# Kernel optimization log

Hardware: AMD Instinct MI355X
Metric: run time of the kernel (lower is better)

Reference implementation:

```python
import jax, jax.numpy as jnp
import numpy as np

# Model dims (DeepSeek-V2-lite style MLA)
B, T, DIM = 1, 2048, 2048
H = 16
NOPE, ROPE, VD = 128, 64, 128
QKD = NOPE + ROPE            # 192
Q_LORA, KV_LORA = 768, 512
EPS = 1e-6
SOFTSCALE = QKD * -0.5       # faithful to source: qk_head_dim * -0.5 == -96.0 (NOT **-0.5)


def rms_norm(x, w):
    # F.rms_norm: x / sqrt(mean(x^2) + eps) * w
    return x * jax.lax.rsqrt(jnp.mean(x * x, axis=-1, keepdims=True) + EPS) * w


def apply_rope(x, freqs):
    # x: [B, T, H, D] with D even; freqs: [T, D//2] rotation angles.
    # Complex-pair rotation on interleaved (even, odd) pairs, DeepSeek style.
    b, t, h, d = x.shape
    xr = x.reshape(b, t, h, d // 2, 2)
    cos = jnp.cos(freqs)[None, :, None, :]
    sin = jnp.sin(freqs)[None, :, None, :]
    x1, x2 = xr[..., 0], xr[..., 1]
    out = jnp.stack([x1 * cos - x2 * sin, x1 * sin + x2 * cos], axis=-1)
    return out.reshape(b, t, h, d)


def setup_inputs() -> dict:
    key = jax.random.key(0)
    ks = jax.random.split(key, 8)

    def w(k, out_f, in_f):
        return jax.random.normal(k, (out_f, in_f), dtype=jnp.float32) * (in_f ** -0.5)

    x = jax.random.normal(ks[0], (B, T, DIM), dtype=jnp.float32)

    # RoPE angles: positions x inv_freq, [T, ROPE//2]
    inv_freq = 1.0 / (10000.0 ** (np.arange(0, ROPE, 2, dtype=np.float32) / ROPE))
    freqs = jnp.asarray(np.outer(np.arange(T, dtype=np.float32), inv_freq))

    # additive causal mask [T, T]
    mask = jnp.where(np.tril(np.ones((T, T), dtype=bool)), 0.0, -jnp.inf).astype(jnp.float32)

    return {
        "x": x,
        "freqs": freqs,
        "mask": mask,
        "wq_a": w(ks[1], Q_LORA, DIM),
        "q_norm_w": jnp.ones((Q_LORA,), dtype=jnp.float32),
        "wq_b": w(ks[2], H * QKD, Q_LORA),
        "wkv_a": w(ks[3], KV_LORA + ROPE, DIM),
        "kv_norm_w": jnp.ones((KV_LORA,), dtype=jnp.float32),
        "wkv_b": w(ks[4], H * (NOPE + VD), KV_LORA),
        "wo": w(ks[5], DIM, H * VD),
    }


def reference(x, freqs, mask, wq_a, q_norm_w, wq_b, wkv_a, kv_norm_w, wkv_b, wo):
    b, t, _ = x.shape

    # low-rank query path: wq_b(rms_norm(wq_a(x)))
    q = rms_norm(x @ wq_a.T, q_norm_w) @ wq_b.T            # [B,T,H*QKD]
    q = q.reshape(b, t, H, QKD)
    q_nope, q_pe = q[..., :NOPE], q[..., NOPE:]
    q_pe = apply_rope(q_pe, freqs)

    # low-rank kv path
    kv_full = x @ wkv_a.T                                  # [B,T,KV_LORA+ROPE]
    c_kv, k_pe = kv_full[..., :KV_LORA], kv_full[..., KV_LORA:]
    k_pe = apply_rope(k_pe[:, :, None, :], freqs)          # [B,T,1,ROPE]
    kv = rms_norm(c_kv, kv_norm_w) @ wkv_b.T               # [B,T,H*(NOPE+VD)]
    kv = kv.reshape(b, t, H, NOPE + VD)
    k_nope, v = kv[..., :NOPE], kv[..., NOPE:]

    qh = jnp.concatenate([q_nope, q_pe], axis=-1)          # [B,T,H,QKD]
    kh = jnp.concatenate([k_nope, jnp.broadcast_to(k_pe, (b, t, H, ROPE))], axis=-1)

    # scores [B,S,H,T]; mask.unsqueeze(1) in torch -> mask[:, None, :] here
    scores = jnp.einsum("bshd,bthd->bsht", qh, kh) * SOFTSCALE
    scores = scores + mask[:, None, :]
    attn = jax.nn.softmax(scores.astype(jnp.float32), axis=-1).astype(x.dtype)

    y = jnp.einsum("bsht,bthd->bshd", attn, v)             # [B,T,H,VD]
    out = y.reshape(b, t, H * VD) @ wo.T                   # [B,T,DIM]
    return out
```

## Files before the change

kernel.cpp:

```cpp
#include <hip/hip_runtime.h>
#include <hip/hip_bf16.h>
#include <math.h>


#define T_DIM 2048
#define HEADS 16
#define D_MODEL 2048
#define NOPE_D 128
#define ROPE_D 64
#define QKD_D 192
#define VD_D 128
#define QLORA 768
#define KVLORA 512
#define KVFULL_D 576
#define SOFTSCALE -96.0f
#define EPS_RMS 1e-6f

typedef __hip_bfloat16 bf;
typedef __attribute__((ext_vector_type(8))) short bf16x8;
typedef __attribute__((ext_vector_type(4))) float f32x4;

#define SLICE_BYTES 16896
#define PART1_CAP 992

#define GLOAD_LDS16(gptr, lptr)                                               \
    __builtin_amdgcn_global_load_lds(                                         \
        (const __attribute__((address_space(1))) unsigned int*)(gptr),        \
        (__attribute__((address_space(3))) unsigned int*)(lptr), 16, 0, 0)

__device__ __forceinline__ void split2(float v, bf* hi, bf* lo) {
    bf h = __float2bfloat16(v);
    *hi = h;
    *lo = __float2bfloat16(v - __bfloat162float(h));
}

__global__ __launch_bounds__(256) void cvt_split(
    const float* __restrict__ in, bf* __restrict__ hi, bf* __restrict__ lo, int n)
{
    const int i = (blockIdx.x * 256 + threadIdx.x) * 4;
    if (i >= n) return;
    float4 v = *(const float4*)&in[i];
    float vv[4] = {v.x, v.y, v.z, v.w};
#pragma unroll
    for (int u = 0; u < 4; u++) split2(vv[u], &hi[i + u], &lo[i + u]);
}

__global__ __launch_bounds__(256) void cvt_hi(
    const float* __restrict__ in, bf* __restrict__ hi, int n)
{
    const int i = (blockIdx.x * 256 + threadIdx.x) * 4;
    if (i >= n) return;
    float4 v = *(const float4*)&in[i];
    hi[i + 0] = __float2bfloat16(v.x);
    hi[i + 1] = __float2bfloat16(v.y);
    hi[i + 2] = __float2bfloat16(v.z);
    hi[i + 3] = __float2bfloat16(v.w);
}

__global__ __launch_bounds__(256) void rmsnorm_cvt(
    const float* __restrict__ in, int ld, int D, const float* __restrict__ w,
    bf* __restrict__ hi, bf* __restrict__ lo)
{
    const int row = blockIdx.x;
    const float* r = in + (size_t)row * ld;
    float ss = 0.0f;
    for (int i = threadIdx.x; i < D; i += 256) { float v = r[i]; ss += v * v; }
#pragma unroll
    for (int o = 32; o > 0; o >>= 1) ss += __shfl_down(ss, o, 64);
    __shared__ float red[4];
    if ((threadIdx.x & 63) == 0) red[threadIdx.x >> 6] = ss;
    __syncthreads();
    ss = red[0] + red[1] + red[2] + red[3];
    const float scale = rsqrtf(ss / (float)D + EPS_RMS);
    for (int i = threadIdx.x; i < D; i += 256) {
        const float v = r[i] * scale * w[i];
        split2(v, &hi[(size_t)row * D + i], &lo[(size_t)row * D + i]);
    }
}

__global__ __launch_bounds__(256) void rope_k_cvt(
    const float* __restrict__ kvfull, const float* __restrict__ freqs,
    bf* __restrict__ kpeh, bf* __restrict__ kpel)
{
    const int idx = blockIdx.x * 256 + threadIdx.x;
    const int i = idx & 31, t = idx >> 5;
    const float f = freqs[t * 32 + i];
    float sn, cs; sincosf(f, &sn, &cs);
    const float x1 = kvfull[(size_t)t * KVFULL_D + KVLORA + 2 * i];
    const float x2 = kvfull[(size_t)t * KVFULL_D + KVLORA + 2 * i + 1];
    split2(x1 * cs - x2 * sn, &kpeh[t * 64 + 2 * i], &kpel[t * 64 + 2 * i]);
    split2(x1 * sn + x2 * cs, &kpeh[t * 64 + 2 * i + 1], &kpel[t * 64 + 2 * i + 1]);
}

__global__ __launch_bounds__(256) void transpose_v(
    const bf* __restrict__ vh, bf* __restrict__ vT)
{
    __shared__ bf s[32][33];
    const int t0 = blockIdx.x * 32, d0 = blockIdx.y * 32, h = blockIdx.z;
    const int tid = threadIdx.x;
    const int i = tid >> 3, j0 = (tid & 7) * 4;
    const bf* src = vh + ((size_t)(t0 + i) * 16 + h) * 128 + d0 + j0;
#pragma unroll
    for (int u = 0; u < 4; u++) s[i][j0 + u] = src[u];
    __syncthreads();
    const int jj = tid >> 3, i0 = (tid & 7) * 4;
    bf* dst = vT + ((size_t)h * 128 + d0 + jj) * 2048 + t0 + i0;
#pragma unroll
    for (int u = 0; u < 4; u++) dst[u] = s[i0 + u][jj];
}

template <int MODE>
__global__ __launch_bounds__(256) void gemm_split(
    const bf* __restrict__ Ah, const bf* __restrict__ Al,
    const bf* __restrict__ Bh, const bf* __restrict__ Bl,
    const float* __restrict__ freqs,
    float* __restrict__ Cf, bf* __restrict__ Oh, bf* __restrict__ Ol,
    bf* __restrict__ O2, int M, int N, int K)
{
    __shared__ bf sAh[128 * 32], sAl[128 * 32];
    __shared__ bf sBh[128 * 32], sBl[128 * 32];

    const int tid = threadIdx.x;
    const int lane = tid & 63, wave = tid >> 6;
    const int row0 = blockIdx.y * 128, col0 = blockIdx.x * 128;
    const int wm = (wave & 1) * 64, wn = (wave >> 1) * 64;
    const int fr = lane & 15, quad = lane >> 4;

    f32x4 acc[4][4];
#pragma unroll
    for (int i = 0; i < 4; i++)
#pragma unroll
        for (int j = 0; j < 4; j++) acc[i][j] = (f32x4){0.f, 0.f, 0.f, 0.f};

    const int trow = tid >> 2;
    const int tcol = (tid & 3) * 8;
    const size_t ldsoff = (size_t)wave * 1024;

    for (int kt = 0; kt < K; kt += 32) {
        __syncthreads();
        GLOAD_LDS16(Ah + (size_t)(row0 + trow) * K + kt + tcol,      (char*)sAh + ldsoff);
        GLOAD_LDS16(Ah + (size_t)(row0 + 64 + trow) * K + kt + tcol, (char*)sAh + 4096 + ldsoff);
        GLOAD_LDS16(Al + (size_t)(row0 + trow) * K + kt + tcol,      (char*)sAl + ldsoff);
        GLOAD_LDS16(Al + (size_t)(row0 + 64 + trow) * K + kt + tcol, (char*)sAl + 4096 + ldsoff);
        GLOAD_LDS16(Bh + (size_t)(col0 + trow) * K + kt + tcol,      (char*)sBh + ldsoff);
        GLOAD_LDS16(Bh + (size_t)(col0 + 64 + trow) * K + kt + tcol, (char*)sBh + 4096 + ldsoff);
        GLOAD_LDS16(Bl + (size_t)(col0 + trow) * K + kt + tcol,      (char*)sBl + ldsoff);
        GLOAD_LDS16(Bl + (size_t)(col0 + 64 + trow) * K + kt + tcol, (char*)sBl + 4096 + ldsoff);
        __syncthreads();

        bf16x8 a_h[4], a_l[4], b_h[4], b_l[4];
#pragma unroll
        for (int mt = 0; mt < 4; mt++) {
            const int r = (wm + mt * 16 + fr) * 32 + quad * 8;
            a_h[mt] = *(const bf16x8*)&sAh[r];
            a_l[mt] = *(const bf16x8*)&sAl[r];
        }
#pragma unroll
        for (int nt = 0; nt < 4; nt++) {
            const int r = (wn + nt * 16 + fr) * 32 + quad * 8;
            b_h[nt] = *(const bf16x8*)&sBh[r];
            b_l[nt] = *(const bf16x8*)&sBl[r];
        }
#pragma unroll
        for (int mt = 0; mt < 4; mt++)
#pragma unroll
            for (int nt = 0; nt < 4; nt++) {
                acc[mt][nt] = __builtin_amdgcn_mfma_f32_16x16x32_bf16(
                    a_l[mt], b_h[nt], acc[mt][nt], 0, 0, 0);
                acc[mt][nt] = __builtin_amdgcn_mfma_f32_16x16x32_bf16(
                    a_h[mt], b_l[nt], acc[mt][nt], 0, 0, 0);
                acc[mt][nt] = __builtin_amdgcn_mfma_f32_16x16x32_bf16(
                    a_h[mt], b_h[nt], acc[mt][nt], 0, 0, 0);
            }
    }

#pragma unroll
    for (int mt = 0; mt < 4; mt++)
#pragma unroll
        for (int nt = 0; nt < 4; nt++) {
            const int colb = col0 + wn + nt * 16;
            const int col = colb + fr;
            if (MODE == 1) {
                const int d0 = colb % 192;
                const bool rope = (d0 >= 128);
                const int ii = (d0 + fr - 128) >> 1;
#pragma unroll
                for (int r = 0; r < 4; r++) {
                    const int row = row0 + wm + mt * 16 + quad * 4 + r;
                    float v = acc[mt][nt][r];
                    if (rope) {
                        const float other = __shfl_xor(v, 1);
                        float sn, cs; sincosf(freqs[row * 32 + ii], &sn, &cs);
                        v = (fr & 1) ? (other * sn + v * cs) : (v * cs - other * sn);
                    }
                    bf h8, l8; split2(v, &h8, &l8);
                    Oh[(size_t)row * N + col] = h8;
                    Ol[(size_t)row * N + col] = l8;
                }
            } else {
                const int hh = col >> 8;
                const int d = col & 255;
#pragma unroll
                for (int r = 0; r < 4; r++) {
                    const int row = row0 + wm + mt * 16 + quad * 4 + r;
                    const float v = acc[mt][nt][r];
                    if (d < 128) {
                        bf h8, l8; split2(v, &h8, &l8);
                        Oh[(size_t)row * 2048 + hh * 128 + d] = h8;
                        Ol[(size_t)row * 2048 + hh * 128 + d] = l8;
                    } else {
                        O2[(size_t)row * 2048 + hh * 128 + (d - 128)] = __float2bfloat16(v);
                    }
                }
            }
        }
}

__global__ __launch_bounds__(256) void gemm_split64(
    const bf* __restrict__ Ah, const bf* __restrict__ Al,
    const bf* __restrict__ Bh, const bf* __restrict__ Bl,
    float* __restrict__ Cf, int M, int N, int K)
{
    __shared__ bf sAh[64 * 32], sAl[64 * 32];
    __shared__ bf sBh[64 * 32], sBl[64 * 32];

    const int tid = threadIdx.x;
    const int lane = tid & 63, wave = tid >> 6;
    const int row0 = blockIdx.y * 64, col0 = blockIdx.x * 64;
    const int wm = (wave & 1) * 32, wn = (wave >> 1) * 32;
    const int fr = lane & 15, quad = lane >> 4;

    f32x4 acc[2][2];
#pragma unroll
    for (int i = 0; i < 2; i++)
#pragma unroll
        for (int j = 0; j < 2; j++) acc[i][j] = (f32x4){0.f, 0.f, 0.f, 0.f};

    const int trow = tid >> 2;
    const int tcol = (tid & 3) * 8;
    const size_t ldsoff = (size_t)wave * 1024;

    for (int kt = 0; kt < K; kt += 32) {
        __syncthreads();
        GLOAD_LDS16(Ah + (size_t)(row0 + trow) * K + kt + tcol, (char*)sAh + ldsoff);
        GLOAD_LDS16(Al + (size_t)(row0 + trow) * K + kt + tcol, (char*)sAl + ldsoff);
        GLOAD_LDS16(Bh + (size_t)(col0 + trow) * K + kt + tcol, (char*)sBh + ldsoff);
        GLOAD_LDS16(Bl + (size_t)(col0 + trow) * K + kt + tcol, (char*)sBl + ldsoff);
        __syncthreads();

        bf16x8 a_h[2], a_l[2], b_h[2], b_l[2];
#pragma unroll
        for (int mt = 0; mt < 2; mt++) {
            const int r = (wm + mt * 16 + fr) * 32 + quad * 8;
            a_h[mt] = *(const bf16x8*)&sAh[r];
            a_l[mt] = *(const bf16x8*)&sAl[r];
        }
#pragma unroll
        for (int nt = 0; nt < 2; nt++) {
            const int r = (wn + nt * 16 + fr) * 32 + quad * 8;
            b_h[nt] = *(const bf16x8*)&sBh[r];
            b_l[nt] = *(const bf16x8*)&sBl[r];
        }
#pragma unroll
        for (int mt = 0; mt < 2; mt++)
#pragma unroll
            for (int nt = 0; nt < 2; nt++) {
                acc[mt][nt] = __builtin_amdgcn_mfma_f32_16x16x32_bf16(
                    a_l[mt], b_h[nt], acc[mt][nt], 0, 0, 0);
                acc[mt][nt] = __builtin_amdgcn_mfma_f32_16x16x32_bf16(
                    a_h[mt], b_l[nt], acc[mt][nt], 0, 0, 0);
                acc[mt][nt] = __builtin_amdgcn_mfma_f32_16x16x32_bf16(
                    a_h[mt], b_h[nt], acc[mt][nt], 0, 0, 0);
            }
    }

#pragma unroll
    for (int mt = 0; mt < 2; mt++)
#pragma unroll
        for (int nt = 0; nt < 2; nt++)
#pragma unroll
            for (int r = 0; r < 4; r++)
                Cf[(size_t)(row0 + wm + mt * 16 + quad * 4 + r) * N +
                   col0 + wn + nt * 16 + fr] = acc[mt][nt][r];
}

__global__ __launch_bounds__(256) void gemm_bf16(
    const bf* __restrict__ Ah, const bf* __restrict__ Bh,
    float* __restrict__ Cf, int M, int N, int K)
{
    __shared__ bf sAh[128 * 32];
    __shared__ bf sBh[128 * 32];

    const int tid = threadIdx.x;
    const int lane = tid & 63, wave = tid >> 6;
    const int row0 = blockIdx.y * 128, col0 = blockIdx.x * 128;
    const int wm = (wave & 1) * 64, wn = (wave >> 1) * 64;
    const int fr = lane & 15, quad = lane >> 4;

    f32x4 acc[4][4];
#pragma unroll
    for (int i = 0; i < 4; i++)
#pragma unroll
        for (int j = 0; j < 4; j++) acc[i][j] = (f32x4){0.f, 0.f, 0.f, 0.f};

    const int trow = tid >> 2;
    const int tcol = (tid & 3) * 8;
    const size_t ldsoff = (size_t)wave * 1024;

    for (int kt = 0; kt < K; kt += 32) {
        __syncthreads();
        GLOAD_LDS16(Ah + (size_t)(row0 + trow) * K + kt + tcol,      (char*)sAh + ldsoff);
        GLOAD_LDS16(Ah + (size_t)(row0 + 64 + trow) * K + kt + tcol, (char*)sAh + 4096 + ldsoff);
        GLOAD_LDS16(Bh + (size_t)(col0 + trow) * K + kt + tcol,      (char*)sBh + ldsoff);
        GLOAD_LDS16(Bh + (size_t)(col0 + 64 + trow) * K + kt + tcol, (char*)sBh + 4096 + ldsoff);
        __syncthreads();

        bf16x8 a_h[4], b_h[4];
#pragma unroll
        for (int mt = 0; mt < 4; mt++)
            a_h[mt] = *(const bf16x8*)&sAh[(wm + mt * 16 + fr) * 32 + quad * 8];
#pragma unroll
        for (int nt = 0; nt < 4; nt++)
            b_h[nt] = *(const bf16x8*)&sBh[(wn + nt * 16 + fr) * 32 + quad * 8];
#pragma unroll
        for (int mt = 0; mt < 4; mt++)
#pragma unroll
            for (int nt = 0; nt < 4; nt++)
                acc[mt][nt] = __builtin_amdgcn_mfma_f32_16x16x32_bf16(
                    a_h[mt], b_h[nt], acc[mt][nt], 0, 0, 0);
    }

#pragma unroll
    for (int mt = 0; mt < 4; mt++)
#pragma unroll
        for (int nt = 0; nt < 4; nt++)
#pragma unroll
            for (int r = 0; r < 4; r++)
                Cf[(size_t)(row0 + wm + mt * 16 + quad * 4 + r) * N +
                   col0 + wn + nt * 16 + fr] = acc[mt][nt][r];
}

__global__ __launch_bounds__(256, 2) void attn_mfma(
    const bf* __restrict__ qh, const bf* __restrict__ ql,
    const bf* __restrict__ knh, const bf* __restrict__ knl,
    const bf* __restrict__ kpeh, const bf* __restrict__ kpel,
    const bf* __restrict__ vT,
    char* __restrict__ part1, char* __restrict__ part2)
{
    const int bid = blockIdx.x;
    const int xcd = bid & 7;
    const int rr8 = bid >> 3;
    const int h = (xcd << 1) | (rr8 & 1);
    const int sidx = rr8 >> 1;
    int qt, s;
    if (sidx < 8)       { qt = sidx; s = 0; }
    else if (sidx < 24) { const int r = sidx - 8;  qt = 8  + (r >> 1); s = r & 1; }
    else if (sidx < 48) { const int r = sidx - 24; qt = 16 + r / 3;    s = r % 3; }
    else                { const int r = sidx - 48; qt = 24 + (r >> 2); s = r & 3; }

    const int tid = threadIdx.x;
    const int lane = tid & 63, wave = tid >> 6;
    const int fr = lane & 15, quad = lane >> 4;
    const int wn = wave * 32;

    __shared__ __align__(16) char smem[35840];
    bf* sQh = (bf*)(smem);
    bf* sQl = (bf*)(smem + 4096);
    bf* sKh = (bf*)(smem + 8192);
    bf* sKl = (bf*)(smem + 16384);
    bf* sVt = (bf*)(smem + 8192);
    bf* Ps  = (bf*)(smem + 24576);
    float* redM = (float*)(smem + 33792);
    float* redS = (float*)(smem + 34816);

    float m_i[16], l_i[16], al[16];
    f32x4 O[4][2];
#pragma unroll
    for (int i = 0; i < 16; i++) { m_i[i] = -INFINITY; l_i[i] = 0.0f; }
#pragma unroll
    for (int mt = 0; mt < 4; mt++)
#pragma unroll
        for (int nt = 0; nt < 2; nt++) O[mt][nt] = (f32x4){0.f, 0.f, 0.f, 0.f};

    const int q0 = qt * 64;
    const int kstart = s * 512;
    const int kend = min(kstart + 512, (qt + 1) * 64);
    const int trow = tid >> 2, tcol = (tid & 3) * 8;
    const size_t loff = (size_t)wave * 1024;

    for (int k0 = kstart; k0 < kend; k0 += 128) {
        f32x4 S[4][2];
#pragma unroll
        for (int mt = 0; mt < 4; mt++)
#pragma unroll
            for (int nt = 0; nt < 2; nt++) S[mt][nt] = (f32x4){0.f, 0.f, 0.f, 0.f};

        for (int ch = 0; ch < 6; ch++) {
            const int d0 = ch * 32;
            __syncthreads();
            GLOAD_LDS16(qh + ((size_t)(q0 + trow) * 16 + h) * 192 + d0 + tcol, (char*)sQh + loff);
            GLOAD_LDS16(ql + ((size_t)(q0 + trow) * 16 + h) * 192 + d0 + tcol, (char*)sQl + loff);
            if (d0 < 128) {
                GLOAD_LDS16(knh + ((size_t)(k0 + trow) * 16 + h) * 128 + d0 + tcol,      (char*)sKh + loff);
                GLOAD_LDS16(knh + ((size_t)(k0 + 64 + trow) * 16 + h) * 128 + d0 + tcol, (char*)sKh + 4096 + loff);
                GLOAD_LDS16(knl + ((size_t)(k0 + trow) * 16 + h) * 128 + d0 + tcol,      (char*)sKl + loff);
                GLOAD_LDS16(knl + ((size_t)(k0 + 64 + trow) * 16 + h) * 128 + d0 + tcol, (char*)sKl + 4096 + loff);
            } else {
                GLOAD_LDS16(kpeh + (size_t)(k0 + trow) * 64 + (d0 - 128) + tcol,      (char*)sKh + loff);
                GLOAD_LDS16(kpeh + (size_t)(k0 + 64 + trow) * 64 + (d0 - 128) + tcol, (char*)sKh + 4096 + loff);
                GLOAD_LDS16(kpel + (size_t)(k0 + trow) * 64 + (d0 - 128) + tcol,      (char*)sKl + loff);
                GLOAD_LDS16(kpel + (size_t)(k0 + 64 + trow) * 64 + (d0 - 128) + tcol, (char*)sKl + 4096 + loff);
            }
            __syncthreads();

            bf16x8 a_h[4], a_l[4], b_h[2], b_l[2];
#pragma unroll
            for (int mt = 0; mt < 4; mt++) {
                const int r = (mt * 16 + fr) * 32 + quad * 8;
                a_h[mt] = *(const bf16x8*)&sQh[r];
                a_l[mt] = *(const bf16x8*)&sQl[r];
            }
#pragma unroll
            for (int nt = 0; nt < 2; nt++) {
                const int r = (wn + nt * 16 + fr) * 32 + quad * 8;
                b_h[nt] = *(const bf16x8*)&sKh[r];
                b_l[nt] = *(const bf16x8*)&sKl[r];
            }
#pragma unroll
            for (int mt = 0; mt < 4; mt++)
#pragma unroll
                for (int nt = 0; nt < 2; nt++) {
                    S[mt][nt] = __builtin_amdgcn_mfma_f32_16x16x32_bf16(
                        a_l[mt], b_h[nt], S[mt][nt], 0, 0, 0);
                    S[mt][nt] = __builtin_amdgcn_mfma_f32_16x16x32_bf16(
                        a_h[mt], b_l[nt], S[mt][nt], 0, 0, 0);
                    S[mt][nt] = __builtin_amdgcn_mfma_f32_16x16x32_bf16(
                        a_h[mt], b_h[nt], S[mt][nt], 0, 0, 0);
                }
        }

#pragma unroll
        for (int mt = 0; mt < 4; mt++)
#pragma unroll
            for (int rr = 0; rr < 4; rr++) {
                const int ri = mt * 16 + quad * 4 + rr;
                const int rowg = q0 + ri;
                float v0 = S[mt][0][rr] * SOFTSCALE;
                float v1 = S[mt][1][rr] * SOFTSCALE;
                if (k0 + wn + fr > rowg)      v0 = -INFINITY;
                if (k0 + wn + 16 + fr > rowg) v1 = -INFINITY;
                S[mt][0][rr] = v0; S[mt][1][rr] = v1;
                float pm = fmaxf(v0, v1);
#pragma unroll
                for (int o = 1; o < 16; o <<= 1) pm = fmaxf(pm, __shfl_xor(pm, o, 64));
                if (fr == 0) redM[ri * 4 + wave] = pm;
            }
        __syncthreads();
#pragma unroll
        for (int mt = 0; mt < 4; mt++)
#pragma unroll
            for (int rr = 0; rr < 4; rr++) {
                const int idx = mt * 4 + rr;
                const int ri = mt * 16 + quad * 4 + rr;
                const float4 g = *(const float4*)&redM[ri * 4];
                const float gm = fmaxf(fmaxf(g.x, g.y), fmaxf(g.z, g.w));
                const float mn = fmaxf(m_i[idx], gm);
                al[idx] = __expf(m_i[idx] - mn);
                m_i[idx] = mn;
                const float p0 = __expf(S[mt][0][rr] - mn);
                const float p1 = __expf(S[mt][1][rr] - mn);
                S[mt][0][rr] = p0; S[mt][1][rr] = p1;
                float ps = p0 + p1;
#pragma unroll
                for (int o = 1; o < 16; o <<= 1) ps += __shfl_xor(ps, o, 64);
                if (fr == 0) redS[ri * 4 + wave] = ps;
            }
#pragma unroll
        for (int mt = 0; mt < 4; mt++)
#pragma unroll
            for (int nt = 0; nt < 2; nt++)
#pragma unroll
                for (int rr = 0; rr < 4; rr++) O[mt][nt][rr] *= al[mt * 4 + rr];
        __syncthreads();
#pragma unroll
        for (int mt = 0; mt < 4; mt++)
#pragma unroll
            for (int rr = 0; rr < 4; rr++) {
                const int idx = mt * 4 + rr;
                const int ri = mt * 16 + quad * 4 + rr;
                const float4 s4 = *(const float4*)&redS[ri * 4];
                l_i[idx] = l_i[idx] * al[idx] + (s4.x + s4.y + s4.z + s4.w);
            }

#pragma unroll
        for (int half = 0; half < 2; half++) {
            if (half) __syncthreads();
            if ((wave >> 1) == half) {
                const int kc = wn - half * 64;
#pragma unroll
                for (int mt = 0; mt < 4; mt++)
#pragma unroll
                    for (int rr = 0; rr < 4; rr++) {
                        const int ri = mt * 16 + quad * 4 + rr;
                        Ps[ri * 72 + kc + fr]      = __float2bfloat16(S[mt][0][rr]);
                        Ps[ri * 72 + kc + 16 + fr] = __float2bfloat16(S[mt][1][rr]);
                    }
            }
            const int kb = k0 + half * 64;
            GLOAD_LDS16(vT + ((size_t)(h * 128 + trow)) * 2048 + kb + tcol,           (char*)sVt + loff);
            GLOAD_LDS16(vT + ((size_t)(h * 128 + 64 + trow)) * 2048 + kb + tcol,      (char*)sVt + 4096 + loff);
            GLOAD_LDS16(vT + ((size_t)(h * 128 + trow)) * 2048 + kb + 32 + tcol,      (char*)sVt + 8192 + loff);
            GLOAD_LDS16(vT + ((size_t)(h * 128 + 64 + trow)) * 2048 + kb + 32 + tcol, (char*)sVt + 12288 + loff);
            __syncthreads();
#pragma unroll
            for (int vc = 0; vc < 2; vc++) {
                bf16x8 ap[4], bv[2];
#pragma unroll
                for (int mt = 0; mt < 4; mt++)
                    ap[mt] = *(const bf16x8*)&Ps[(mt * 16 + fr) * 72 + vc * 32 + quad * 8];
#pragma unroll
                for (int nt = 0; nt < 2; nt++)
                    bv[nt] = *(const bf16x8*)&sVt[vc * 4096 + (wn + nt * 16 + fr) * 32 + quad * 8];
#pragma unroll
                for (int mt = 0; mt < 4; mt++)
#pragma unroll
                    for (int nt = 0; nt < 2; nt++)
                        O[mt][nt] = __builtin_amdgcn_mfma_f32_16x16x32_bf16(
                            ap[mt], bv[nt], O[mt][nt], 0, 0, 0);
            }
        }
    }

    const int g = h * 80 + sidx;
    char* base = (g < PART1_CAP) ? part1 + (size_t)g * SLICE_BYTES
                                 : part2 + (size_t)(g - PART1_CAP) * SLICE_BYTES;
    bf* Op = (bf*)base;
    float* mp = (float*)(base + 16384);
    float* lp = (float*)(base + 16640);
#pragma unroll
    for (int mt = 0; mt < 4; mt++)
#pragma unroll
        for (int rr = 0; rr < 4; rr++) {
            const int idx = mt * 4 + rr;
            const int ri = mt * 16 + quad * 4 + rr;
#pragma unroll
            for (int nt = 0; nt < 2; nt++)
                Op[ri * 128 + wn + nt * 16 + fr] = __float2bfloat16(O[mt][nt][rr]);
            if (wave == 0 && fr == 0) { mp[ri] = m_i[idx]; lp[ri] = l_i[idx]; }
        }
}

__global__ __launch_bounds__(256) void attn_merge(
    const char* __restrict__ part1, const char* __restrict__ part2,
    bf* __restrict__ yh)
{
    const int h = blockIdx.x & 15, qt = blockIdx.x >> 4;
    const int a = qt >> 3, b = qt & 7;
    const int sidx0 = 4 * a * (a + 1) + b * (a + 1);
    const int nst = a + 1;
    const int tid = threadIdx.x;
    const int r = tid >> 2;
    const int c0 = (tid & 3) * 32;

    const char* bases[4];
    float m_s[4], l_s[4];
    for (int s = 0; s < nst; s++) {
        const int g = h * 80 + sidx0 + s;
        bases[s] = (g < PART1_CAP) ? part1 + (size_t)g * SLICE_BYTES
                                   : part2 + (size_t)(g - PART1_CAP) * SLICE_BYTES;
        m_s[s] = ((const float*)(bases[s] + 16384))[r];
        l_s[s] = ((const float*)(bases[s] + 16640))[r];
    }
    float M = -INFINITY;
    for (int s = 0; s < nst; s++) M = fmaxf(M, m_s[s]);
    float denom = 0.0f;
    for (int s = 0; s < nst; s++) denom += __expf(m_s[s] - M) * l_s[s];
    float w[4];
    for (int s = 0; s < nst; s++) w[s] = __expf(m_s[s] - M) / denom;

    const int row = qt * 64 + r;
    bf* dst = yh + ((size_t)row * 16 + h) * 128 + c0;
#pragma unroll
    for (int cc = 0; cc < 32; cc += 8) {
        float acc[8] = {0, 0, 0, 0, 0, 0, 0, 0};
        for (int s = 0; s < nst; s++) {
            const bf16x8 ov = *(const bf16x8*)((const bf*)bases[s] + r * 128 + c0 + cc);
#pragma unroll
            for (int u = 0; u < 8; u++) {
                union { short s16; bf b16; } cv; cv.s16 = ov[u];
                acc[u] += w[s] * __bfloat162float(cv.b16);
            }
        }
#pragma unroll
        for (int u = 0; u < 8; u++) dst[cc + u] = __float2bfloat16(acc[u]);
    }
}

extern "C" void kernel_launch(void* const* d_in, const int* in_sizes, int n_in,
                              void* d_out, int out_size, void* d_ws, size_t ws_size,
                              hipStream_t stream)
{
    const float* x        = (const float*)d_in[0];
    const float* freqs    = (const float*)d_in[1];
    const float* wq_a     = (const float*)d_in[3];
    const float* q_norm_w = (const float*)d_in[4];
    const float* wq_b     = (const float*)d_in[5];
    const float* wkv_a    = (const float*)d_in[6];
    const float* kv_norm_w= (const float*)d_in[7];
    const float* wkv_b    = (const float*)d_in[8];
    const float* wo       = (const float*)d_in[9];
    float* out            = (float*)d_out;

    char* ws = (char*)d_ws;
    bf* xh = (bf*)(ws);
    bf* xl = (bf*)(ws + 8388608);
    bf* yh = (bf*)(ws);
    bf* vT = (bf*)(ws + 8388608);
    char* AR = ws + 16777216;
    bf*    wah    = (bf*)(AR);
    bf*    wal    = (bf*)(AR + 3145728);
    float* qa     = (float*)(AR + 6291456);
    bf*    qah    = (bf*)(AR);
    bf*    qal    = (bf*)(AR + 3145728);
    bf*    wbh    = (bf*)(AR + 6291456);
    bf*    wbl    = (bf*)(AR + 11010048);
    bf*    kah    = (bf*)(AR);
    bf*    kal    = (bf*)(AR + 2359296);
    float* kvfull = (float*)(AR + 4718592);
    bf*    ckvh   = (bf*)(AR + 9437184);
    bf*    ckvl   = (bf*)(AR + 11534336);
    bf*    wvh    = (bf*)(AR);
    bf*    wvl    = (bf*)(AR + 4194304);
    char*  part1  = AR;
    bf*    woh    = (bf*)(AR);
    bf* qh   = (bf*)(ws + 33554432);
    bf* ql   = (bf*)(ws + 46137344);
    bf* knh  = (bf*)(ws + 58720256);
    bf* knl  = (bf*)(ws + 67108864);
    bf* vh   = (bf*)(ws + 75497472);
    char* part2 = ws + 75497472;
    bf* kpeh = (bf*)(ws + 83886080);
    bf* kpel = (bf*)(ws + 84148224);

    dim3 blk(256);

    cvt_split<<<4096, blk, 0, stream>>>(x, xh, xl, D_MODEL * D_MODEL);
    cvt_split<<<1536, blk, 0, stream>>>(wq_a, wah, wal, QLORA * D_MODEL);
    gemm_split64<<<dim3(12, 32), blk, 0, stream>>>(
        xh, xl, wah, wal, qa, T_DIM, QLORA, D_MODEL);
    rmsnorm_cvt<<<T_DIM, blk, 0, stream>>>(qa, QLORA, QLORA, q_norm_w, qah, qal);
    cvt_split<<<2304, blk, 0, stream>>>(wq_b, wbh, wbl, 3072 * QLORA);
    gemm_split<1><<<dim3(24, 16), blk, 0, stream>>>(
        qah, qal, wbh, wbl, freqs, nullptr, qh, ql, nullptr,
        T_DIM, 3072, QLORA);
    cvt_split<<<1152, blk, 0, stream>>>(wkv_a, kah, kal, KVFULL_D * D_MODEL);
    gemm_split64<<<dim3(9, 32), blk, 0, stream>>>(
        xh, xl, kah, kal, kvfull, T_DIM, KVFULL_D, D_MODEL);
    rope_k_cvt<<<256, blk, 0, stream>>>(kvfull, freqs, kpeh, kpel);
    rmsnorm_cvt<<<T_DIM, blk, 0, stream>>>(kvfull, KVFULL_D, KVLORA, kv_norm_w, ckvh, ckvl);
    cvt_split<<<2048, blk, 0, stream>>>(wkv_b, wvh, wvl, 4096 * KVLORA);
    gemm_split<2><<<dim3(32, 16), blk, 0, stream>>>(
        ckvh, ckvl, wvh, wvl, nullptr, nullptr, knh, knl, vh,
        T_DIM, 4096, KVLORA);
    transpose_v<<<dim3(64, 4, 16), blk, 0, stream>>>(vh, vT);
    attn_mfma<<<dim3(1280), blk, 0, stream>>>(
        qh, ql, knh, knl, kpeh, kpel, vT, part1, part2);
    attn_merge<<<dim3(512), blk, 0, stream>>>(part1, part2, yh);
    cvt_hi<<<4096, blk, 0, stream>>>(wo, woh, D_MODEL * D_MODEL);
    gemm_bf16<<<dim3(16, 16), blk, 0, stream>>>(
        yh, woh, out, T_DIM, D_MODEL, D_MODEL);
}
```

Before: 728.2 us.

## Drop split-K attention with merge; double-buffer QK loads and order tiles longest-first

Replaces the split-KV attention (1280 blocks writing partial O/m/l plus a separate merge kernel) with one block per (head, query tile) that walks the full causal key range and normalizes in-kernel, writing yh directly. Query tiles are scheduled longest-first to balance the causal workload. The QK chunk loop now uses two LDS buffers so the next chunk's global-to-LDS load is issued before the barrier, cutting one sync per chunk. LDS grows to about 60 KB, which may lower occupancy, and only 512 blocks may leave CUs underused during the long tiles.

New measurement: 650.5 us. 10.7% less time.

```diff
diff --git a/kernel.cpp b/kernel.cpp
--- a/kernel.cpp
+++ b/kernel.cpp
@@ -19,9 +19,6 @@
 typedef __hip_bfloat16 bf;
 typedef __attribute__((ext_vector_type(8))) short bf16x8;
 typedef __attribute__((ext_vector_type(4))) float f32x4;
-
-#define SLICE_BYTES 16896
-#define PART1_CAP 992
 
 #define GLOAD_LDS16(gptr, lptr)                                               \
     __builtin_amdgcn_global_load_lds(                                         \
@@ -344,34 +341,21 @@
     const bf* __restrict__ qh, const bf* __restrict__ ql,
     const bf* __restrict__ knh, const bf* __restrict__ knl,
     const bf* __restrict__ kpeh, const bf* __restrict__ kpel,
-    const bf* __restrict__ vT,
-    char* __restrict__ part1, char* __restrict__ part2)
+    const bf* __restrict__ vT, bf* __restrict__ yh)
 {
     const int bid = blockIdx.x;
-    const int xcd = bid & 7;
-    const int rr8 = bid >> 3;
-    const int h = (xcd << 1) | (rr8 & 1);
-    const int sidx = rr8 >> 1;
-    int qt, s;
-    if (sidx < 8)       { qt = sidx; s = 0; }
-    else if (sidx < 24) { const int r = sidx - 8;  qt = 8  + (r >> 1); s = r & 1; }
-    else if (sidx < 48) { const int r = sidx - 24; qt = 16 + r / 3;    s = r % 3; }
-    else                { const int r = sidx - 48; qt = 24 + (r >> 2); s = r & 3; }
+    const int h = bid & 15;
+    const int qt = (bid < 256) ? (31 - (bid >> 4)) : ((bid - 256) >> 4);
 
     const int tid = threadIdx.x;
     const int lane = tid & 63, wave = tid >> 6;
     const int fr = lane & 15, quad = lane >> 4;
     const int wn = wave * 32;
 
-    __shared__ __align__(16) char smem[35840];
-    bf* sQh = (bf*)(smem);
-    bf* sQl = (bf*)(smem + 4096);
-    bf* sKh = (bf*)(smem + 8192);
-    bf* sKl = (bf*)(smem + 16384);
-    bf* sVt = (bf*)(smem + 8192);
-    bf* Ps  = (bf*)(smem + 24576);
-    float* redM = (float*)(smem + 33792);
-    float* redS = (float*)(smem + 34816);
+    __shared__ __align__(16) char smem[60416];
+    bf* Ps  = (bf*)(smem + 49152);
+    float* redM = (float*)(smem + 58368);
+    float* redS = (float*)(smem + 59392);
 
     float m_i[16], l_i[16], al[16];
     f32x4 O[4][2];
@@ -383,36 +367,42 @@
         for (int nt = 0; nt < 2; nt++) O[mt][nt] = (f32x4){0.f, 0.f, 0.f, 0.f};
 
     const int q0 = qt * 64;
-    const int kstart = s * 512;
-    const int kend = min(kstart + 512, (qt + 1) * 64);
+    const int nkt = ((qt + 1) * 64 + 127) >> 7;
     const int trow = tid >> 2, tcol = (tid & 3) * 8;
     const size_t loff = (size_t)wave * 1024;
 
-    for (int k0 = kstart; k0 < kend; k0 += 128) {
+    for (int kt = 0; kt < nkt; kt++) {
+        const int k0 = kt * 128;
         f32x4 S[4][2];
 #pragma unroll
         for (int mt = 0; mt < 4; mt++)
 #pragma unroll
             for (int nt = 0; nt < 2; nt++) S[mt][nt] = (f32x4){0.f, 0.f, 0.f, 0.f};
+
+        __syncthreads();
 
         for (int ch = 0; ch < 6; ch++) {
             const int d0 = ch * 32;
+            char* buf = smem + ((ch & 1) ? 24576 : 0);
+            GLOAD_LDS16(qh + ((size_t)(q0 + trow) * 16 + h) * 192 + d0 + tcol, buf + loff);
+            GLOAD_LDS16(ql + ((size_t)(q0 + trow) * 16 + h) * 192 + d0 + tcol, buf + 4096 + loff);
+            if (d0 < 128) {
+                GLOAD_LDS16(knh + ((size_t)(k0 + trow) * 16 + h) * 128 + d0 + tcol,      buf + 8192 + loff);
+                GLOAD_LDS16(knh + ((size_t)(k0 + 64 + trow) * 16 + h) * 128 + d0 + tcol, buf + 12288 + loff);
+                GLOAD_LDS16(knl + ((size_t)(k0 + trow) * 16 + h) * 128 + d0 + tcol,      buf + 16384 + loff);
+                GLOAD_LDS16(knl + ((size_t)(k0 + 64 + trow) * 16 + h) * 128 + d0 + tcol, buf + 20480 + loff);
+            } else {
+                GLOAD_LDS16(kpeh + (size_t)(k0 + trow) * 64 + (d0 - 128) + tcol,      buf + 8192 + loff);
+                GLOAD_LDS16(kpeh + (size_t)(k0 + 64 + trow) * 64 + (d0 - 128) + tcol, buf + 12288 + loff);
+                GLOAD_LDS16(kpel + (size_t)(k0 + trow) * 64 + (d0 - 128) + tcol,      buf + 16384 + loff);
+                GLOAD_LDS16(kpel + (size_t)(k0 + 64 + trow) * 64 + (d0 - 128) + tcol, buf + 20480 + loff);
+            }
             __syncthreads();
-            GLOAD_LDS16(qh + ((size_t)(q0 + trow) * 16 + h) * 192 + d0 + tcol, (char*)sQh + loff);
-            GLOAD_LDS16(ql + ((size_t)(q0 + trow) * 16 + h) * 192 + d0 + tcol, (char*)sQl + loff);
-            if (d0 < 128) {
-                GLOAD_LDS16(knh + ((size_t)(k0 + trow) * 16 + h) * 128 + d0 + tcol,      (char*)sKh + loff);
-                GLOAD_LDS16(knh + ((size_t)(k0 + 64 + trow) * 16 + h) * 128 + d0 + tcol, (char*)sKh + 4096 + loff);
-                GLOAD_LDS16(knl + ((size_t)(k0 + trow) * 16 + h) * 128 + d0 + tcol,      (char*)sKl + loff);
-                GLOAD_LDS16(knl + ((size_t)(k0 + 64 + trow) * 16 + h) * 128 + d0 + tcol, (char*)sKl + 4096 + loff);
-            } else {
-                GLOAD_LDS16(kpeh + (size_t)(k0 + trow) * 64 + (d0 - 128) + tcol,      (char*)sKh + loff);
-                GLOAD_LDS16(kpeh + (size_t)(k0 + 64 + trow) * 64 + (d0 - 128) + tcol, (char*)sKh + 4096 + loff);
-                GLOAD_LDS16(kpel + (size_t)(k0 + trow) * 64 + (d0 - 128) + tcol,      (char*)sKl + loff);
-                GLOAD_LDS16(kpel + (size_t)(k0 + 64 + trow) * 64 + (d0 - 128) + tcol, (char*)sKl + 4096 + loff);
-            }
-            __syncthreads();
-
+
+            const bf* sQh = (const bf*)buf;
+            const bf* sQl = (const bf*)(buf + 4096);
+            const bf* sKh = (const bf*)(buf + 8192);
+            const bf* sKl = (const bf*)(buf + 16384);
             bf16x8 a_h[4], a_l[4], b_h[2], b_l[2];
 #pragma unroll
             for (int mt = 0; mt < 4; mt++) {
@@ -492,6 +482,7 @@
                 l_i[idx] = l_i[idx] * al[idx] + (s4.x + s4.y + s4.z + s4.w);
             }
 
+        bf* sVt = (bf*)smem;
 #pragma unroll
         for (int half = 0; half < 2; half++) {
             if (half) __syncthreads();
@@ -531,69 +522,17 @@
         }
     }
 
-    const int g = h * 80 + sidx;
-    char* base = (g < PART1_CAP) ? part1 + (size_t)g * SLICE_BYTES
-                                 : part2 + (size_t)(g - PART1_CAP) * SLICE_BYTES;
-    bf* Op = (bf*)base;
-    float* mp = (float*)(base + 16384);
-    float* lp = (float*)(base + 16640);
 #pragma unroll
     for (int mt = 0; mt < 4; mt++)
 #pragma unroll
         for (int rr = 0; rr < 4; rr++) {
-            const int idx = mt * 4 + rr;
-            const int ri = mt * 16 + quad * 4 + rr;
+            const float inv = 1.0f / l_i[mt * 4 + rr];
+            const int row = q0 + mt * 16 + quad * 4 + rr;
 #pragma unroll
             for (int nt = 0; nt < 2; nt++)
-                Op[ri * 128 + wn + nt * 16 + fr] = __float2bfloat16(O[mt][nt][rr]);
-            if (wave == 0 && fr == 0) { mp[ri] = m_i[idx]; lp[ri] = l_i[idx]; }
-        }
-}
-
-__global__ __launch_bounds__(256) void attn_merge(
-    const char* __restrict__ part1, const char* __restrict__ part2,
-    bf* __restrict__ yh)
-{
-    const int h = blockIdx.x & 15, qt = blockIdx.x >> 4;
-    const int a = qt >> 3, b = qt & 7;
-    const int sidx0 = 4 * a * (a + 1) + b * (a + 1);
-    const int nst = a + 1;
-    const int tid = threadIdx.x;
-    const int r = tid >> 2;
-    const int c0 = (tid & 3) * 32;
-
-    const char* bases[4];
-    float m_s[4], l_s[4];
-    for (int s = 0; s < nst; s++) {
-        const int g = h * 80 + sidx0 + s;
-        bases[s] = (g < PART1_CAP) ? part1 + (size_t)g * SLICE_BYTES
-                                   : part2 + (size_t)(g - PART1_CAP) * SLICE_BYTES;
-        m_s[s] = ((const float*)(bases[s] + 16384))[r];
-        l_s[s] = ((const float*)(bases[s] + 16640))[r];
-    }
-    float M = -INFINITY;
-    for (int s = 0; s < nst; s++) M = fmaxf(M, m_s[s]);
-    float denom = 0.0f;
-    for (int s = 0; s < nst; s++) denom += __expf(m_s[s] - M) * l_s[s];
-    float w[4];
-    for (int s = 0; s < nst; s++) w[s] = __expf(m_s[s] - M) / denom;
-
-    const int row = qt * 64 + r;
-    bf* dst = yh + ((size_t)row * 16 + h) * 128 + c0;
-#pragma unroll
-    for (int cc = 0; cc < 32; cc += 8) {
-        float acc[8] = {0, 0, 0, 0, 0, 0, 0, 0};
-        for (int s = 0; s < nst; s++) {
-            const bf16x8 ov = *(const bf16x8*)((const bf*)bases[s] + r * 128 + c0 + cc);
-#pragma unroll
-            for (int u = 0; u < 8; u++) {
-                union { short s16; bf b16; } cv; cv.s16 = ov[u];
-                acc[u] += w[s] * __bfloat162float(cv.b16);
-            }
-        }
-#pragma unroll
-        for (int u = 0; u < 8; u++) dst[cc + u] = __float2bfloat16(acc[u]);
-    }
+                yh[((size_t)row * 16 + h) * 128 + wn + nt * 16 + fr] =
+                    __float2bfloat16(O[mt][nt][rr] * inv);
+        }
 }
 
 extern "C" void kernel_launch(void* const* d_in, const int* in_sizes, int n_in,
@@ -631,14 +570,12 @@
     bf*    ckvl   = (bf*)(AR + 11534336);
     bf*    wvh    = (bf*)(AR);
     bf*    wvl    = (bf*)(AR + 4194304);
-    char*  part1  = AR;
     bf*    woh    = (bf*)(AR);
     bf* qh   = (bf*)(ws + 33554432);
     bf* ql   = (bf*)(ws + 46137344);
     bf* knh  = (bf*)(ws + 58720256);
     bf* knl  = (bf*)(ws + 67108864);
     bf* vh   = (bf*)(ws + 75497472);
-    char* part2 = ws + 75497472;
     bf* kpeh = (bf*)(ws + 83886080);
     bf* kpel = (bf*)(ws + 84148224);
 
@@ -663,9 +600,8 @@
         ckvh, ckvl, wvh, wvl, nullptr, nullptr, knh, knl, vh,
         T_DIM, 4096, KVLORA);
     transpose_v<<<dim3(64, 4, 16), blk, 0, stream>>>(vh, vT);
-    attn_mfma<<<dim3(1280), blk, 0, stream>>>(
-        qh, ql, knh, knl, kpeh, kpel, vT, part1, part2);
-    attn_merge<<<dim3(512), blk, 0, stream>>>(part1, part2, yh);
+    attn_mfma<<<dim3(512), blk, 0, stream>>>(
+        qh, ql, knh, knl, kpeh, kpel, vT, yh);
     cvt_hi<<<4096, blk, 0, stream>>>(wo, woh, D_MODEL * D_MODEL);
     gemm_bf16<<<dim3(16, 16), blk, 0, stream>>>(
         yh, woh, out, T_DIM, D_MODEL, D_MODEL);
```
